# Kernel tuning notes

Hardware: AMD Instinct MI355X
Metric: run time of the kernel (lower is better)

Reference implementation:

```python
import jax, jax.numpy as jnp
import numpy as np

H = 256
EPS = 1e-5
WIN = (-2, -1, 1, 2)  # radius_graph(pos/2^(d+1), k=2) on unit-spaced timestamps


def leaky(x):
    return jnp.where(x >= 0, x, 0.2 * x)


def layernorm(x, g, b):
    mu = jnp.mean(x, axis=-1, keepdims=True)
    var = jnp.mean(jnp.square(x - mu), axis=-1, keepdims=True)
    return (x - mu) * jax.lax.rsqrt(var + EPS) * g + b


def nbr_mean(x, offsets):
    # mean over temporal-window neighbors within each video row; [B,T,C]
    if not offsets:
        return jnp.zeros_like(x)
    T = x.shape[1]
    idx = jnp.arange(T)
    acc = jnp.zeros_like(x)
    cnt = jnp.zeros((T,), x.dtype)
    for o in offsets:
        valid = (idx + o >= 0) & (idx + o < T)
        acc = acc + jnp.where(valid[None, :, None], jnp.roll(x, -o, axis=1), 0.0)
        cnt = cnt + valid.astype(x.dtype)
    return acc / jnp.maximum(cnt, 1.0)[None, :, None]


def conv(x, Ws, Wn, b, offsets):
    # GraphConv with mean aggregation: W_self x_i + W_nbr mean_j x_j + b
    return x @ Ws + nbr_mean(x, offsets) @ Wn + b


def stage(x, s, Wself, Wnbr, bconv, ln_g, ln_b, offsets):
    # Dropout(eval)=id; conv; LeakyReLU(0.2); conv; LayerNorm; LeakyReLU(0.2)
    x = leaky(conv(x, Wself[s, 0], Wnbr[s, 0], bconv[s, 0], offsets))
    x = conv(x, Wself[s, 1], Wnbr[s, 1], bconv[s, 1], offsets)
    return leaky(layernorm(x, ln_g[s], ln_b[s]))


def upsample2(c):
    # knn_interpolate(k=2) from coarse (stride-2 subsampled) grid back to fine grid:
    # even fine nodes coincide with a coarse node (dist 0 -> weight ~inf -> copy);
    # odd fine nodes are equidistant from two coarse nodes (0.5/0.5), except the
    # last odd node whose 2-NN are at dist s and 3s -> weights 0.9/0.1.
    even = c
    nxt = jnp.concatenate([c[:, 1:], c[:, -1:]], axis=1)
    odd = 0.5 * (c + nxt)
    odd = odd.at[:, -1].set(0.9 * c[:, -1] + 0.1 * c[:, -2])
    B, Tc, C = c.shape
    return jnp.stack([even, odd], axis=2).reshape(B, 2 * Tc, C)


def setup_inputs() -> dict:
    key = jax.random.key(0)
    ks = jax.random.split(key, 8)
    B, T, F = 16, 4096, 1024
    N = B * T
    x = jax.random.normal(ks[0], (N, 1, F), dtype=jnp.float32)
    pos = (jnp.arange(N) % T).astype(jnp.float32)
    batch = (jnp.arange(N) // T).astype(jnp.int64)
    indices = (jnp.arange(N) % T).astype(jnp.int64)
    Wp = jax.random.normal(ks[1], (F, H), dtype=jnp.float32) / np.sqrt(F)
    bp = jnp.zeros((H,), jnp.float32)
    Wself = jax.random.normal(ks[2], (6, 2, H, H), dtype=jnp.float32) / np.sqrt(H)
    Wnbr = jax.random.normal(ks[3], (6, 2, H, H), dtype=jnp.float32) / np.sqrt(H)
    bconv = jnp.zeros((6, 2, H), jnp.float32)
    ln_g = jnp.ones((6, H), jnp.float32)
    ln_b = jnp.zeros((6, H), jnp.float32)
    return {"x": x, "pos": pos, "batch": batch, "indices": indices, "B": B, "T": T,
            "Wp": Wp, "bp": bp, "Wself": Wself, "Wnbr": Wnbr, "bconv": bconv,
            "ln_g": ln_g, "ln_b": ln_b}


def reference(x, pos, batch, indices, B, T, Wp, bp, Wself, Wnbr, bconv, ln_g, ln_b):
    # input projection: Rearrange 'B S F -> B (S F)' (S=1) + Linear
    feat = x.reshape(B, T, -1) @ Wp + bp  # [B,T,H]
    # ---- Temporal Encoder ----
    f = feat
    skips = [feat]  # depth-0 input graph features
    for d in range(3):
        f = f[:, ::2]  # batch_subsampling time pooling (stride 2)
        f = f + stage(f, d, Wself, Wnbr, bconv, ln_g, ln_b, WIN)
        if d < 2:
            skips.append(f)
    # ---- Function-Aware Decoder (eval path: clustering_at_inference=False) ----
    for i in range(3):
        res = skips[2 - i]
        f = res + upsample2(f)  # knn_interpolate(k=2) + skip
        dep = 2 - i
        # radius_graph(indices, 1.5): pooled index spacing 2^dep > 1.5 for dep>=1 -> no edges
        offs = WIN if dep == 0 else ()
        f = stage(f, 3 + i, Wself, Wnbr, bconv, ln_g, ln_b, offs)
    return f  # finest-resolution decoder output [B,T,H]
```

## Files before the change

kernel.cpp:

```cpp
#include <hip/hip_runtime.h>

#define HH 256

typedef __attribute__((ext_vector_type(8))) short short8;
typedef __attribute__((ext_vector_type(4))) float f32x4;
typedef __attribute__((ext_vector_type(4))) unsigned short u16x4;
typedef __attribute__((ext_vector_type(8))) unsigned short u16x8;

constexpr int NBATCH = 16;
constexpr int T0   = 4096;
constexpr int FDIM = 1024;
constexpr int R0   = NBATCH * T0;
constexpr int R1   = R0 / 2;
constexpr int R2   = R0 / 4;
constexpr int R3   = R0 / 8;

__device__ __forceinline__ float b2f(unsigned short u) {
    union { unsigned int i; float f; } v; v.i = ((unsigned int)u) << 16; return v.f;
}
__device__ __forceinline__ unsigned short f2b(float f) {
    union { float f; unsigned int i; } v; v.f = f;
    unsigned int r = v.i + 0x7fffu + ((v.i >> 16) & 1u);
    return (unsigned short)(r >> 16);
}
__device__ __forceinline__ void gload16(const void* g, void* l) {
    __builtin_amdgcn_global_load_lds((const __attribute__((address_space(1))) void*)g,
                                     (__attribute__((address_space(3))) void*)l, 16, 0, 0);
}
__device__ __forceinline__ int swz_ks(int chunk)        { return (chunk & 3) ^ ((chunk >> 3) & 3); }
__device__ __forceinline__ int frag_idx(int row, int g) { return (row * 4 + (g ^ ((row >> 1) & 3))) * 8; }

__global__ void transpose_w(const float* __restrict__ src, unsigned short* __restrict__ dst,
                            int K, int tilesPerMat)
{
    int bid = blockIdx.x;
    int m = bid / tilesPerMat;
    int t = bid % tilesPerMat;
    int tr = t >> 3, tc = t & 7;
    const float* S = src + (size_t)m * K * HH;
    unsigned short* D = dst + (size_t)m * HH * K;
    __shared__ float tile[32][33];
    int x = threadIdx.x & 31, y = threadIdx.x >> 5;
#pragma unroll
    for (int i = y; i < 32; i += 8)
        tile[i][x] = S[(size_t)(tr * 32 + i) * HH + tc * 32 + x];
    __syncthreads();
#pragma unroll
    for (int i = y; i < 32; i += 8)
        D[(size_t)(tc * 32 + i) * K + tr * 32 + x] = f2b(tile[x][i]);
}

template<int AMODE, int NBR, int LEAKY>
__launch_bounds__(512)
__global__ void conv_gemm(const unsigned short* __restrict__ A,
                          const unsigned short* __restrict__ Cc,
                          const unsigned short* __restrict__ Bself,
                          const unsigned short* __restrict__ Bnbr,
                          const float* __restrict__ bias,
                          unsigned short* __restrict__ out,
                          int Tl, int Tc, int tlshift)
{
    __shared__ unsigned short As[2][128 * 32];
    __shared__ unsigned short Bs[2][256 * 32];
    const int tid  = threadIdx.x;
    const int lane = tid & 63;
    const int w    = tid >> 6;
    const int wm   = w & 1, wn = w >> 1;
    const long row0 = (long)blockIdx.x * 128;

    const int arr = tid >> 2;
    const int akk = swz_ks(tid);
    const long gr = row0 + arr;

    float ca = 0.f, cb = 0.f; size_t rc0 = 0, rc1 = 0;
    if (AMODE == 2) {
        int t = (int)(gr & (long)(Tl - 1));
        long bq = gr >> tlshift;
        int k = t >> 1;
        rc0 = (size_t)bq * Tc + k;
        if (!(t & 1))        { ca = 1.0f; cb = 0.0f; rc1 = rc0; }
        else if (k < Tc - 1) { ca = 0.5f; cb = 0.5f; rc1 = rc0 + 1; }
        else                 { ca = 0.9f; cb = 0.1f; rc1 = rc0 - 1; }
    }
    int vmask = 0; float vinv = 1.f;
    size_t nrow0 = 0, nrow1 = 0, nrow2 = 0, nrow3 = 0;
    if (NBR) {
        const int offs[4] = {-2, -1, 1, 2};
        int t = (int)(gr & (long)(Tl - 1));
        int cnt = 0;
        size_t nr[4] = {0, 0, 0, 0};
#pragma unroll
        for (int oi = 0; oi < 4; oi++) {
            int tn = t + offs[oi];
            if (tn >= 0 && tn < Tl) {
                vmask |= 1 << oi; cnt++;
                long r = gr + offs[oi];
                nr[oi] = (size_t)((AMODE == 1) ? 2 * r : r) * HH;
            }
        }
        vinv = 1.f / (float)cnt;
        nrow0 = nr[0]; nrow1 = nr[1]; nrow2 = nr[2]; nrow3 = nr[3];
    }

    f32x4 acc[4][4] = {};
    u16x8 pv0 = {}, pv1 = {}, pv2 = {}, pv3 = {};

    const int NT = NBR ? 16 : 8;

    auto issue = [&](int t, int b) {
        const int seg = NBR ? (t >> 3) : 0;
        const int k0 = (t & 7) * 32;
        const unsigned short* __restrict__ Bm = (NBR && seg) ? Bnbr : Bself;
        gload16(Bm + (size_t)arr * HH + k0 + akk * 8,        &Bs[b][tid * 8]);
        gload16(Bm + (size_t)(128 + arr) * HH + k0 + akk * 8, &Bs[b][(tid + 512) * 8]);
        if (seg == 0) {
            if (AMODE == 0) {
                gload16(A + (size_t)gr * HH + k0 + akk * 8, &As[b][tid * 8]);
            } else if (AMODE == 1) {
                gload16(A + (size_t)(2 * gr) * HH + k0 + akk * 8, &As[b][tid * 8]);
            } else {
                pv0 = *(const u16x8*)(A + (size_t)gr * HH + k0 + akk * 8);
                pv1 = *(const u16x8*)(Cc + rc0 * HH + k0 + akk * 8);
                pv2 = *(const u16x8*)(Cc + rc1 * HH + k0 + akk * 8);
            }
        } else {
            if (vmask & 1) pv0 = *(const u16x8*)(A + nrow0 + k0 + akk * 8);
            if (vmask & 2) pv1 = *(const u16x8*)(A + nrow1 + k0 + akk * 8);
            if (vmask & 4) pv2 = *(const u16x8*)(A + nrow2 + k0 + akk * 8);
            if (vmask & 8) pv3 = *(const u16x8*)(A + nrow3 + k0 + akk * 8);
        }
    };
    auto finish = [&](int t, int b) {
        const int seg = NBR ? (t >> 3) : 0;
        if (seg == 0) {
            if (AMODE == 2) {
                u16x8 o;
#pragma unroll
                for (int j = 0; j < 8; j++)
                    o[j] = f2b(b2f(pv0[j]) + ca * b2f(pv1[j]) + cb * b2f(pv2[j]));
                *(u16x8*)&As[b][tid * 8] = o;
            }
        } else {
            float a8[8] = {0, 0, 0, 0, 0, 0, 0, 0};
            if (vmask & 1) {
#pragma unroll
                for (int j = 0; j < 8; j++) a8[j] += b2f(pv0[j]);
            }
            if (vmask & 2) {
#pragma unroll
                for (int j = 0; j < 8; j++) a8[j] += b2f(pv1[j]);
            }
            if (vmask & 4) {
#pragma unroll
                for (int j = 0; j < 8; j++) a8[j] += b2f(pv2[j]);
            }
            if (vmask & 8) {
#pragma unroll
                for (int j = 0; j < 8; j++) a8[j] += b2f(pv3[j]);
            }
            u16x8 o;
#pragma unroll
            for (int j = 0; j < 8; j++) o[j] = f2b(a8[j] * vinv);
            *(u16x8*)&As[b][tid * 8] = o;
        }
    };

    issue(0, 0);
    finish(0, 0);
    __syncthreads();

    int buf = 0;
#pragma unroll
    for (int t = 0; t < NT; ++t) {
        if (t + 1 < NT) issue(t + 1, buf ^ 1);

        short8 af[4], bg[4];
#pragma unroll
        for (int i = 0; i < 4; i++) {
            af[i] = *(const short8*)&As[buf][frag_idx(wm * 64 + i * 16 + (lane & 15), lane >> 4)];
            bg[i] = *(const short8*)&Bs[buf][frag_idx(wn * 64 + i * 16 + (lane & 15), lane >> 4)];
        }
#pragma unroll
        for (int mi = 0; mi < 4; mi++)
#pragma unroll
            for (int ni = 0; ni < 4; ni++)
                acc[mi][ni] = __builtin_amdgcn_mfma_f32_16x16x32_bf16(af[mi], bg[ni], acc[mi][ni], 0, 0, 0);

        if (t + 1 < NT) {
            finish(t + 1, buf ^ 1);
            __syncthreads();
            buf ^= 1;
        }
    }

#pragma unroll
    for (int mi = 0; mi < 4; mi++) {
        size_t rbase = (size_t)row0 + wm * 64 + mi * 16 + (lane >> 4) * 4;
#pragma unroll
        for (int ni = 0; ni < 4; ni++) {
            int c = wn * 64 + ni * 16 + (lane & 15);
            float bb = bias[c];
            f32x4 v = acc[mi][ni];
#pragma unroll
            for (int r = 0; r < 4; r++) {
                float t = v[r] + bb;
                if (LEAKY) t = (t >= 0.f) ? t : 0.2f * t;
                out[(rbase + r) * HH + c] = f2b(t);
            }
        }
    }
}

__launch_bounds__(512)
__global__ void proj_gemm(const float* __restrict__ A, const unsigned short* __restrict__ Bt,
                          const float* __restrict__ bias, unsigned short* __restrict__ out)
{
    __shared__ unsigned short As[2][128 * 32];
    __shared__ unsigned short Bs[2][256 * 32];
    const int tid  = threadIdx.x;
    const int lane = tid & 63;
    const int w    = tid >> 6;
    const int wm   = w & 1, wn = w >> 1;
    const size_t row0 = (size_t)blockIdx.x * 128;

    const int arr = tid >> 2;
    const int akk = swz_ks(tid);

    f32x4 acc[4][4] = {};
    float4 pa0, pa1;

    const int NT = FDIM / 32;

    auto issue = [&](int t, int b) {
        const int k0 = t * 32;
        gload16(Bt + (size_t)arr * FDIM + k0 + akk * 8,         &Bs[b][tid * 8]);
        gload16(Bt + (size_t)(128 + arr) * FDIM + k0 + akk * 8, &Bs[b][(tid + 512) * 8]);
        const float* s = A + (row0 + arr) * (size_t)FDIM + k0 + akk * 8;
        pa0 = *(const float4*)s;
        pa1 = *(const float4*)(s + 4);
    };
    auto finish = [&](int t, int b) {
        u16x8 o = { f2b(pa0.x), f2b(pa0.y), f2b(pa0.z), f2b(pa0.w),
                    f2b(pa1.x), f2b(pa1.y), f2b(pa1.z), f2b(pa1.w) };
        *(u16x8*)&As[b][tid * 8] = o;
    };

    issue(0, 0);
    finish(0, 0);
    __syncthreads();

    int buf = 0;
    for (int t = 0; t < NT; ++t) {
        if (t + 1 < NT) issue(t + 1, buf ^ 1);

        short8 af[4], bg[4];
#pragma unroll
        for (int i = 0; i < 4; i++) {
            af[i] = *(const short8*)&As[buf][frag_idx(wm * 64 + i * 16 + (lane & 15), lane >> 4)];
            bg[i] = *(const short8*)&Bs[buf][frag_idx(wn * 64 + i * 16 + (lane & 15), lane >> 4)];
        }
#pragma unroll
        for (int mi = 0; mi < 4; mi++)
#pragma unroll
            for (int ni = 0; ni < 4; ni++)
                acc[mi][ni] = __builtin_amdgcn_mfma_f32_16x16x32_bf16(af[mi], bg[ni], acc[mi][ni], 0, 0, 0);

        if (t + 1 < NT) {
            finish(t + 1, buf ^ 1);
            __syncthreads();
            buf ^= 1;
        }
    }

#pragma unroll
    for (int mi = 0; mi < 4; mi++) {
        size_t rbase = row0 + wm * 64 + mi * 16 + (lane >> 4) * 4;
#pragma unroll
        for (int ni = 0; ni < 4; ni++) {
            int c = wn * 64 + ni * 16 + (lane & 15);
            float bb = bias[c];
            f32x4 v = acc[mi][ni];
#pragma unroll
            for (int r = 0; r < 4; r++)
                out[(rbase + r) * HH + c] = f2b(v[r] + bb);
        }
    }
}

__global__ void upsample_add_kernel(unsigned short* __restrict__ res, const unsigned short* __restrict__ c,
                                    int Tc, int tlshift, int Rout)
{
    int idx = blockIdx.x * 256 + threadIdx.x;
    int r = idx >> 5, cc = (idx & 31) * 8;
    if (r >= Rout) return;
    int Tl = Tc * 2;
    int t  = r & (Tl - 1);
    int bq = r >> tlshift;
    int k  = t >> 1;
    size_t rc = (size_t)bq * Tc + k;
    float u[8];
    if (!(t & 1)) {
        u16x8 v = *(const u16x8*)(c + rc * HH + cc);
#pragma unroll
        for (int j = 0; j < 8; j++) u[j] = b2f(v[j]);
    } else if (k < Tc - 1) {
        u16x8 v0 = *(const u16x8*)(c + rc * HH + cc);
        u16x8 v1 = *(const u16x8*)(c + (rc + 1) * HH + cc);
#pragma unroll
        for (int j = 0; j < 8; j++) u[j] = 0.5f * (b2f(v0[j]) + b2f(v1[j]));
    } else {
        u16x8 v0 = *(const u16x8*)(c + rc * HH + cc);
        u16x8 vm = *(const u16x8*)(c + (rc - 1) * HH + cc);
#pragma unroll
        for (int j = 0; j < 8; j++) u[j] = 0.9f * b2f(v0[j]) + 0.1f * b2f(vm[j]);
    }
    u16x8 rv = *(const u16x8*)(res + (size_t)r * HH + cc);
    u16x8 o;
#pragma unroll
    for (int j = 0; j < 8; j++) o[j] = f2b(b2f(rv[j]) + u[j]);
    *(u16x8*)(res + (size_t)r * HH + cc) = o;
}

template<int MODE>
__launch_bounds__(256)
__global__ void ln_kernel(const unsigned short* __restrict__ src, void* __restrict__ dstv,
                          const unsigned short* __restrict__ prev,
                          const float* __restrict__ g, const float* __restrict__ b)
{
    size_t row = (size_t)blockIdx.x * 4 + (threadIdx.x >> 6);
    int lane = threadIdx.x & 63;
    u16x4 xv = *(const u16x4*)(src + row * HH + lane * 4);
    float x0 = b2f(xv[0]), x1 = b2f(xv[1]), x2 = b2f(xv[2]), x3 = b2f(xv[3]);

    float s = x0 + x1 + x2 + x3;
#pragma unroll
    for (int off = 32; off >= 1; off >>= 1) s += __shfl_xor(s, off);
    float mu = s * (1.0f / HH);

    float d0 = x0 - mu, d1 = x1 - mu, d2 = x2 - mu, d3 = x3 - mu;
    float vs = d0 * d0 + d1 * d1 + d2 * d2 + d3 * d3;
#pragma unroll
    for (int off = 32; off >= 1; off >>= 1) vs += __shfl_xor(vs, off);
    float inv = rsqrtf(vs * (1.0f / HH) + 1e-5f);

    float4 gv = *reinterpret_cast<const float4*>(g + lane * 4);
    float4 bv = *reinterpret_cast<const float4*>(b + lane * 4);
    float y0 = d0 * inv * gv.x + bv.x;
    float y1 = d1 * inv * gv.y + bv.y;
    float y2 = d2 * inv * gv.z + bv.z;
    float y3 = d3 * inv * gv.w + bv.w;
    y0 = (y0 >= 0.f) ? y0 : 0.2f * y0;
    y1 = (y1 >= 0.f) ? y1 : 0.2f * y1;
    y2 = (y2 >= 0.f) ? y2 : 0.2f * y2;
    y3 = (y3 >= 0.f) ? y3 : 0.2f * y3;

    if (MODE == 2) {
        float* d = (float*)dstv + row * HH + lane * 4;
        *reinterpret_cast<float4*>(d) = make_float4(y0, y1, y2, y3);
    } else {
        if (MODE == 1) {
            u16x4 rv = *(const u16x4*)(prev + (2 * row) * HH + lane * 4);
            y0 += b2f(rv[0]); y1 += b2f(rv[1]); y2 += b2f(rv[2]); y3 += b2f(rv[3]);
        }
        unsigned short* d = (unsigned short*)dstv + row * HH + lane * 4;
        u16x4 o = { f2b(y0), f2b(y1), f2b(y2), f2b(y3) };
        *(u16x4*)d = o;
    }
}

extern "C" void kernel_launch(void* const* d_in, const int* in_sizes, int n_in,
                              void* d_out, int out_size, void* d_ws, size_t ws_size,
                              hipStream_t stream)
{
    const float* x     = (const float*)d_in[0];
    const float* Wp    = (const float*)d_in[6];
    const float* bp    = (const float*)d_in[7];
    const float* Wself = (const float*)d_in[8];
    const float* Wnbr  = (const float*)d_in[9];
    const float* bconv = (const float*)d_in[10];
    const float* ln_g  = (const float*)d_in[11];
    const float* ln_b  = (const float*)d_in[12];
    float* out = (float*)d_out;

    char* p = (char*)d_ws;
    unsigned short* Wself_t = (unsigned short*)p; p += (size_t)12 * HH * HH * 2;
    unsigned short* Wnbr_t  = (unsigned short*)p; p += (size_t)12 * HH * HH * 2;
    unsigned short* Wp_t    = (unsigned short*)p; p += (size_t)HH * FDIM * 2;
    unsigned short* c0 = (unsigned short*)p; p += (size_t)R0 * HH * 2;
    unsigned short* c1 = (unsigned short*)p; p += (size_t)R1 * HH * 2;
    unsigned short* c2 = (unsigned short*)p; p += (size_t)R2 * HH * 2;
    unsigned short* c3 = (unsigned short*)p; p += (size_t)R3 * HH * 2;
    unsigned short* t1 = (unsigned short*)p; p += (size_t)R0 * HH * 2;
    unsigned short* t2 = (unsigned short*)p; p += (size_t)R0 * HH * 2;
    if (ws_size < (size_t)(p - (char*)d_ws)) return;

    auto Ws = [&](int i) { return Wself_t + (size_t)i * HH * HH; };
    auto Wn = [&](int i) { return Wnbr_t  + (size_t)i * HH * HH; };

    transpose_w<<<12 * 64, 256, 0, stream>>>(Wself, Wself_t, HH, 64);
    transpose_w<<<12 * 64, 256, 0, stream>>>(Wnbr,  Wnbr_t,  HH, 64);
    transpose_w<<<256, 256, 0, stream>>>(Wp, Wp_t, FDIM, 256);

    proj_gemm<<<R0 / 128, 512, 0, stream>>>(x, Wp_t, bp, c0);

    conv_gemm<1, 1, 1><<<R1 / 128, 512, 0, stream>>>(c0, nullptr, Ws(0), Wn(0), bconv + 0 * HH, t1, 2048, 0, 0);
    conv_gemm<0, 1, 0><<<R1 / 128, 512, 0, stream>>>(t1, nullptr, Ws(1), Wn(1), bconv + 1 * HH, t2, 2048, 0, 0);
    ln_kernel<1><<<R1 / 4, 256, 0, stream>>>(t2, c1, c0, ln_g + 0 * HH, ln_b + 0 * HH);

    conv_gemm<1, 1, 1><<<R2 / 128, 512, 0, stream>>>(c1, nullptr, Ws(2), Wn(2), bconv + 2 * HH, t1, 1024, 0, 0);
    conv_gemm<0, 1, 0><<<R2 / 128, 512, 0, stream>>>(t1, nullptr, Ws(3), Wn(3), bconv + 3 * HH, t2, 1024, 0, 0);
    ln_kernel<1><<<R2 / 4, 256, 0, stream>>>(t2, c2, c1, ln_g + 1 * HH, ln_b + 1 * HH);

    conv_gemm<1, 1, 1><<<R3 / 128, 512, 0, stream>>>(c2, nullptr, Ws(4), Wn(4), bconv + 4 * HH, t1, 512, 0, 0);
    conv_gemm<0, 1, 0><<<R3 / 128, 512, 0, stream>>>(t1, nullptr, Ws(5), Wn(5), bconv + 5 * HH, t2, 512, 0, 0);
    ln_kernel<1><<<R3 / 4, 256, 0, stream>>>(t2, c3, c2, ln_g + 2 * HH, ln_b + 2 * HH);

    conv_gemm<2, 0, 1><<<R2 / 128, 512, 0, stream>>>(c2, c3, Ws(6), nullptr, bconv + 6 * HH, t1, 1024, 512, 10);
    conv_gemm<0, 0, 0><<<R2 / 128, 512, 0, stream>>>(t1, nullptr, Ws(7), nullptr, bconv + 7 * HH, t2, 1024, 0, 0);
    ln_kernel<0><<<R2 / 4, 256, 0, stream>>>(t2, c2, nullptr, ln_g + 3 * HH, ln_b + 3 * HH);
    conv_gemm<2, 0, 1><<<R1 / 128, 512, 0, stream>>>(c1, c2, Ws(8), nullptr, bconv + 8 * HH, t1, 2048, 1024, 11);
    conv_gemm<0, 0, 0><<<R1 / 128, 512, 0, stream>>>(t1, nullptr, Ws(9), nullptr, bconv + 9 * HH, t2, 2048, 0, 0);
    ln_kernel<0><<<R1 / 4, 256, 0, stream>>>(t2, c1, nullptr, ln_g + 4 * HH, ln_b + 4 * HH);
    upsample_add_kernel<<<R0 / 8, 256, 0, stream>>>(c0, c1, 2048, 12, R0);
    conv_gemm<0, 1, 1><<<R0 / 128, 512, 0, stream>>>(c0, nullptr, Ws(10), Wn(10), bconv + 10 * HH, t1, 4096, 0, 0);
    conv_gemm<0, 1, 0><<<R0 / 128, 512, 0, stream>>>(t1, nullptr, Ws(11), Wn(11), bconv + 11 * HH, t2, 4096, 0, 0);
    ln_kernel<2><<<R0 / 4, 256, 0, stream>>>(t2, out, nullptr, ln_g + 5 * HH, ln_b + 5 * HH);
}
```

Before: 430.5 us.

## Fuse LayerNorm into second conv GEMM epilogue and triple-buffer K pipeline

Removes the standalone LayerNorm kernel by computing row mean and variance in the second conv GEMM's epilogue, using cross-lane shuffles plus a small LDS reduction across the four N-waves. The residual add and final fp32 output are written directly, which drops the t2 intermediate round trip. GEMM mainloops move from double to triple buffering with explicit vmcnt waits and raw barriers, and raise wave priority around the MFMA block. Neighbour gathers become branchless by clamping indices and applying validity coefficients. Risks include higher LDS use lowering occupancy, a single-pass variance formula that can lose precision, and brittle hand-written waitcnt counts.

```diff
diff --git a/kernel.cpp b/kernel.cpp
--- a/kernel.cpp
+++ b/kernel.cpp
@@ -27,8 +27,22 @@
     __builtin_amdgcn_global_load_lds((const __attribute__((address_space(1))) void*)g,
                                      (__attribute__((address_space(3))) void*)l, 16, 0, 0);
 }
+__device__ __forceinline__ void barrier_sync() {
+    asm volatile("s_waitcnt lgkmcnt(0)\n\ts_barrier" ::: "memory");
+}
+__device__ __forceinline__ void wait_vm(int n) {
+    switch (n) {
+    case 3: asm volatile("s_waitcnt vmcnt(3)" ::: "memory"); break;
+    case 4: asm volatile("s_waitcnt vmcnt(4)" ::: "memory"); break;
+    case 5: asm volatile("s_waitcnt vmcnt(5)" ::: "memory"); break;
+    case 6: asm volatile("s_waitcnt vmcnt(6)" ::: "memory"); break;
+    default: asm volatile("s_waitcnt vmcnt(0)" ::: "memory"); break;
+    }
+}
 __device__ __forceinline__ int swz_ks(int chunk)        { return (chunk & 3) ^ ((chunk >> 3) & 3); }
 __device__ __forceinline__ int frag_idx(int row, int g) { return (row * 4 + (g ^ ((row >> 1) & 3))) * 8; }
+
+struct PVv { u16x8 v0, v1, v2, v3; };
 
 __global__ void transpose_w(const float* __restrict__ src, unsigned short* __restrict__ dst,
                             int K, int tilesPerMat)
@@ -50,18 +64,24 @@
         D[(size_t)(tc * 32 + i) * K + tr * 32 + x] = f2b(tile[x][i]);
 }
 
-template<int AMODE, int NBR, int LEAKY>
+template<int AMODE, int NBR, int LNFUSE, int OUT>
 __launch_bounds__(512)
-__global__ void conv_gemm(const unsigned short* __restrict__ A,
-                          const unsigned short* __restrict__ Cc,
-                          const unsigned short* __restrict__ Bself,
-                          const unsigned short* __restrict__ Bnbr,
-                          const float* __restrict__ bias,
-                          unsigned short* __restrict__ out,
-                          int Tl, int Tc, int tlshift)
+__global__ void conv_fused(const unsigned short* __restrict__ A,
+                           const unsigned short* __restrict__ Cc,
+                           const unsigned short* __restrict__ prev,
+                           const unsigned short* __restrict__ Bself,
+                           const unsigned short* __restrict__ Bnbr,
+                           const float* __restrict__ bias,
+                           const float* __restrict__ lng,
+                           const float* __restrict__ lnb,
+                           void* __restrict__ dstv,
+                           int Tl, int Tc, int tlshift)
 {
-    __shared__ unsigned short As[2][128 * 32];
-    __shared__ unsigned short Bs[2][256 * 32];
+    constexpr int NT = NBR ? 16 : 8;
+    __shared__ unsigned short As[3][128 * 32];
+    __shared__ unsigned short Bs[3][256 * 32];
+    __shared__ float lnred[LNFUSE ? 128 : 1][8];
+
     const int tid  = threadIdx.x;
     const int lane = tid & 63;
     const int w    = tid >> 6;
@@ -82,130 +102,200 @@
         else if (k < Tc - 1) { ca = 0.5f; cb = 0.5f; rc1 = rc0 + 1; }
         else                 { ca = 0.9f; cb = 0.1f; rc1 = rc0 - 1; }
     }
-    int vmask = 0; float vinv = 1.f;
+    float vinv = 1.f;
+    float cf0 = 0.f, cf1 = 0.f, cf2 = 0.f, cf3 = 0.f;
     size_t nrow0 = 0, nrow1 = 0, nrow2 = 0, nrow3 = 0;
     if (NBR) {
         const int offs[4] = {-2, -1, 1, 2};
         int t = (int)(gr & (long)(Tl - 1));
         int cnt = 0;
-        size_t nr[4] = {0, 0, 0, 0};
+        float cf[4]; size_t nr[4];
 #pragma unroll
         for (int oi = 0; oi < 4; oi++) {
             int tn = t + offs[oi];
-            if (tn >= 0 && tn < Tl) {
-                vmask |= 1 << oi; cnt++;
-                long r = gr + offs[oi];
-                nr[oi] = (size_t)((AMODE == 1) ? 2 * r : r) * HH;
-            }
+            bool v = (tn >= 0 && tn < Tl);
+            cnt += v ? 1 : 0;
+            int tcl = tn < 0 ? 0 : (tn > Tl - 1 ? Tl - 1 : tn);
+            long r = gr - t + tcl;
+            nr[oi] = (size_t)((AMODE == 1) ? 2 * r : r) * HH;
+            cf[oi] = v ? 1.f : 0.f;
         }
         vinv = 1.f / (float)cnt;
+        cf0 = cf[0]; cf1 = cf[1]; cf2 = cf[2]; cf3 = cf[3];
         nrow0 = nr[0]; nrow1 = nr[1]; nrow2 = nr[2]; nrow3 = nr[3];
     }
 
     f32x4 acc[4][4] = {};
-    u16x8 pv0 = {}, pv1 = {}, pv2 = {}, pv3 = {};
-
-    const int NT = NBR ? 16 : 8;
-
-    auto issue = [&](int t, int b) {
-        const int seg = NBR ? (t >> 3) : 0;
+    PVv pvE = {}, pvO = {};
+
+    auto Lof = [&](int t) -> int {
+        const int seg = (NBR && t >= 8) ? 1 : 0;
+        return seg ? 6 : (AMODE == 2 ? 5 : 3);
+    };
+    auto issueB = [&](int t) {
+        const int seg = (NBR && t >= 8) ? 1 : 0;
         const int k0 = (t & 7) * 32;
-        const unsigned short* __restrict__ Bm = (NBR && seg) ? Bnbr : Bself;
-        gload16(Bm + (size_t)arr * HH + k0 + akk * 8,        &Bs[b][tid * 8]);
-        gload16(Bm + (size_t)(128 + arr) * HH + k0 + akk * 8, &Bs[b][(tid + 512) * 8]);
+        const int sl = t % 3;
+        const unsigned short* __restrict__ Bm = seg ? Bnbr : Bself;
+        gload16(Bm + (size_t)arr * HH + k0 + akk * 8,         &Bs[sl][tid * 8]);
+        gload16(Bm + (size_t)(128 + arr) * HH + k0 + akk * 8, &Bs[sl][(tid + 512) * 8]);
+    };
+    auto issueA = [&](int t, PVv& pv) {
+        const int seg = (NBR && t >= 8) ? 1 : 0;
+        const int k0 = (t & 7) * 32;
+        const int sl = t % 3;
         if (seg == 0) {
             if (AMODE == 0) {
-                gload16(A + (size_t)gr * HH + k0 + akk * 8, &As[b][tid * 8]);
+                gload16(A + (size_t)gr * HH + k0 + akk * 8, &As[sl][tid * 8]);
             } else if (AMODE == 1) {
-                gload16(A + (size_t)(2 * gr) * HH + k0 + akk * 8, &As[b][tid * 8]);
+                gload16(A + (size_t)(2 * gr) * HH + k0 + akk * 8, &As[sl][tid * 8]);
             } else {
-                pv0 = *(const u16x8*)(A + (size_t)gr * HH + k0 + akk * 8);
-                pv1 = *(const u16x8*)(Cc + rc0 * HH + k0 + akk * 8);
-                pv2 = *(const u16x8*)(Cc + rc1 * HH + k0 + akk * 8);
+                pv.v0 = *(const u16x8*)(A + (size_t)gr * HH + k0 + akk * 8);
+                pv.v1 = *(const u16x8*)(Cc + rc0 * HH + k0 + akk * 8);
+                pv.v2 = *(const u16x8*)(Cc + rc1 * HH + k0 + akk * 8);
             }
         } else {
-            if (vmask & 1) pv0 = *(const u16x8*)(A + nrow0 + k0 + akk * 8);
-            if (vmask & 2) pv1 = *(const u16x8*)(A + nrow1 + k0 + akk * 8);
-            if (vmask & 4) pv2 = *(const u16x8*)(A + nrow2 + k0 + akk * 8);
-            if (vmask & 8) pv3 = *(const u16x8*)(A + nrow3 + k0 + akk * 8);
-        }
-    };
-    auto finish = [&](int t, int b) {
-        const int seg = NBR ? (t >> 3) : 0;
+            pv.v0 = *(const u16x8*)(A + nrow0 + k0 + akk * 8);
+            pv.v1 = *(const u16x8*)(A + nrow1 + k0 + akk * 8);
+            pv.v2 = *(const u16x8*)(A + nrow2 + k0 + akk * 8);
+            pv.v3 = *(const u16x8*)(A + nrow3 + k0 + akk * 8);
+        }
+    };
+    auto finishA = [&](int t, PVv& pv) {
+        const int seg = (NBR && t >= 8) ? 1 : 0;
+        const int sl = t % 3;
         if (seg == 0) {
             if (AMODE == 2) {
                 u16x8 o;
 #pragma unroll
                 for (int j = 0; j < 8; j++)
-                    o[j] = f2b(b2f(pv0[j]) + ca * b2f(pv1[j]) + cb * b2f(pv2[j]));
-                *(u16x8*)&As[b][tid * 8] = o;
+                    o[j] = f2b(b2f(pv.v0[j]) + ca * b2f(pv.v1[j]) + cb * b2f(pv.v2[j]));
+                *(u16x8*)&As[sl][tid * 8] = o;
             }
         } else {
-            float a8[8] = {0, 0, 0, 0, 0, 0, 0, 0};
-            if (vmask & 1) {
-#pragma unroll
-                for (int j = 0; j < 8; j++) a8[j] += b2f(pv0[j]);
-            }
-            if (vmask & 2) {
-#pragma unroll
-                for (int j = 0; j < 8; j++) a8[j] += b2f(pv1[j]);
-            }
-            if (vmask & 4) {
-#pragma unroll
-                for (int j = 0; j < 8; j++) a8[j] += b2f(pv2[j]);
-            }
-            if (vmask & 8) {
-#pragma unroll
-                for (int j = 0; j < 8; j++) a8[j] += b2f(pv3[j]);
-            }
             u16x8 o;
 #pragma unroll
-            for (int j = 0; j < 8; j++) o[j] = f2b(a8[j] * vinv);
-            *(u16x8*)&As[b][tid * 8] = o;
-        }
-    };
-
-    issue(0, 0);
-    finish(0, 0);
-    __syncthreads();
-
-    int buf = 0;
+            for (int j = 0; j < 8; j++) {
+                float a = cf0 * b2f(pv.v0[j]) + cf1 * b2f(pv.v1[j])
+                        + cf2 * b2f(pv.v2[j]) + cf3 * b2f(pv.v3[j]);
+                o[j] = f2b(a * vinv);
+            }
+            *(u16x8*)&As[sl][tid * 8] = o;
+        }
+    };
+
+    issueB(0); issueA(0, pvE);
+    issueB(1); issueA(1, pvO);
+    wait_vm(Lof(1));
+    finishA(0, pvE);
+    barrier_sync();
+
 #pragma unroll
     for (int t = 0; t < NT; ++t) {
-        if (t + 1 < NT) issue(t + 1, buf ^ 1);
-
+        if (t + 2 < NT) {
+            issueB(t + 2);
+            if (((t + 2) & 1) == 0) issueA(t + 2, pvE); else issueA(t + 2, pvO);
+        }
+
+        const int sl = t % 3;
+        __builtin_amdgcn_s_setprio(1);
         short8 af[4], bg[4];
 #pragma unroll
         for (int i = 0; i < 4; i++) {
-            af[i] = *(const short8*)&As[buf][frag_idx(wm * 64 + i * 16 + (lane & 15), lane >> 4)];
-            bg[i] = *(const short8*)&Bs[buf][frag_idx(wn * 64 + i * 16 + (lane & 15), lane >> 4)];
+            af[i] = *(const short8*)&As[sl][frag_idx(wm * 64 + i * 16 + (lane & 15), lane >> 4)];
+            bg[i] = *(const short8*)&Bs[sl][frag_idx(wn * 64 + i * 16 + (lane & 15), lane >> 4)];
         }
 #pragma unroll
         for (int mi = 0; mi < 4; mi++)
 #pragma unroll
             for (int ni = 0; ni < 4; ni++)
                 acc[mi][ni] = __builtin_amdgcn_mfma_f32_16x16x32_bf16(af[mi], bg[ni], acc[mi][ni], 0, 0, 0);
+        __builtin_amdgcn_s_setprio(0);
 
         if (t + 1 < NT) {
-            finish(t + 1, buf ^ 1);
-            __syncthreads();
-            buf ^= 1;
-        }
-    }
-
-#pragma unroll
-    for (int mi = 0; mi < 4; mi++) {
-        size_t rbase = (size_t)row0 + wm * 64 + mi * 16 + (lane >> 4) * 4;
+            wait_vm((t + 2 < NT) ? Lof(t + 2) : 0);
+            if (((t + 1) & 1) == 0) finishA(t + 1, pvE); else finishA(t + 1, pvO);
+            barrier_sync();
+        }
+    }
+
+    if (LNFUSE == 0) {
+        unsigned short* outp = (unsigned short*)dstv;
+#pragma unroll
+        for (int mi = 0; mi < 4; mi++) {
+            size_t rbase = (size_t)row0 + wm * 64 + mi * 16 + (lane >> 4) * 4;
+#pragma unroll
+            for (int ni = 0; ni < 4; ni++) {
+                int c = wn * 64 + ni * 16 + (lane & 15);
+                float bb = bias[c];
+                f32x4 v = acc[mi][ni];
+#pragma unroll
+                for (int r = 0; r < 4; r++) {
+                    float t = v[r] + bb;
+                    t = (t >= 0.f) ? t : 0.2f * t;
+                    outp[(rbase + r) * HH + c] = f2b(t);
+                }
+            }
+        }
+    } else {
+        float bb[4];
+#pragma unroll
+        for (int ni = 0; ni < 4; ni++) bb[ni] = bias[wn * 64 + ni * 16 + (lane & 15)];
+
+#pragma unroll
+        for (int mi = 0; mi < 4; mi++) {
+#pragma unroll
+            for (int r = 0; r < 4; r++) {
+                float s = 0.f, q = 0.f;
+#pragma unroll
+                for (int ni = 0; ni < 4; ni++) {
+                    float v = acc[mi][ni][r] + bb[ni];
+                    s += v; q += v * v;
+                }
+                s += __shfl_xor(s, 1); q += __shfl_xor(q, 1);
+                s += __shfl_xor(s, 2); q += __shfl_xor(q, 2);
+                s += __shfl_xor(s, 4); q += __shfl_xor(q, 4);
+                s += __shfl_xor(s, 8); q += __shfl_xor(q, 8);
+                if ((lane & 15) == 0) {
+                    int row = wm * 64 + mi * 16 + (lane >> 4) * 4 + r;
+                    lnred[row][wn]     = s;
+                    lnred[row][4 + wn] = q;
+                }
+            }
+        }
+        __syncthreads();
+
+        float gv[4], bv[4];
 #pragma unroll
         for (int ni = 0; ni < 4; ni++) {
             int c = wn * 64 + ni * 16 + (lane & 15);
-            float bb = bias[c];
-            f32x4 v = acc[mi][ni];
+            gv[ni] = lng[c]; bv[ni] = lnb[c];
+        }
+
+#pragma unroll
+        for (int mi = 0; mi < 4; mi++) {
 #pragma unroll
             for (int r = 0; r < 4; r++) {
-                float t = v[r] + bb;
-                if (LEAKY) t = (t >= 0.f) ? t : 0.2f * t;
-                out[(rbase + r) * HH + c] = f2b(t);
+                int row = wm * 64 + mi * 16 + (lane >> 4) * 4 + r;
+                float s = lnred[row][0] + lnred[row][1] + lnred[row][2] + lnred[row][3];
+                float q = lnred[row][4] + lnred[row][5] + lnred[row][6] + lnred[row][7];
+                float mu  = s * (1.0f / HH);
+                float var = q * (1.0f / HH) - mu * mu;
+                float inv = rsqrtf(var + 1e-5f);
+                size_t grow = (size_t)row0 + row;
+#pragma unroll
+                for (int ni = 0; ni < 4; ni++) {
+                    int c = wn * 64 + ni * 16 + (lane & 15);
+                    float v = acc[mi][ni][r] + bb[ni];
+                    float y = (v - mu) * inv * gv[ni] + bv[ni];
+                    y = (y >= 0.f) ? y : 0.2f * y;
+                    if (OUT == 2) {
+                        ((float*)dstv)[grow * HH + c] = y;
+                    } else {
+                        if (OUT == 1) y += b2f(prev[(2 * grow) * HH + c]);
+                        ((unsigned short*)dstv)[grow * HH + c] = f2b(y);
+                    }
+                }
             }
         }
     }
@@ -215,8 +305,9 @@
 __global__ void proj_gemm(const float* __restrict__ A, const unsigned short* __restrict__ Bt,
                           const float* __restrict__ bias, unsigned short* __restrict__ out)
 {
-    __shared__ unsigned short As[2][128 * 32];
-    __shared__ unsigned short Bs[2][256 * 32];
+    constexpr int NT = FDIM / 32;
+    __shared__ unsigned short As[3][128 * 32];
+    __shared__ unsigned short Bs[3][256 * 32];
     const int tid  = threadIdx.x;
     const int lane = tid & 63;
     const int w    = tid >> 6;
@@ -227,48 +318,55 @@
     const int akk = swz_ks(tid);
 
     f32x4 acc[4][4] = {};
-    float4 pa0, pa1;
-
-    const int NT = FDIM / 32;
-
-    auto issue = [&](int t, int b) {
+    float4 paE0, paE1, paO0, paO1;
+
+    auto issue = [&](int t, float4& p0, float4& p1) {
         const int k0 = t * 32;
-        gload16(Bt + (size_t)arr * FDIM + k0 + akk * 8,         &Bs[b][tid * 8]);
-        gload16(Bt + (size_t)(128 + arr) * FDIM + k0 + akk * 8, &Bs[b][(tid + 512) * 8]);
+        const int sl = t % 3;
+        gload16(Bt + (size_t)arr * FDIM + k0 + akk * 8,         &Bs[sl][tid * 8]);
+        gload16(Bt + (size_t)(128 + arr) * FDIM + k0 + akk * 8, &Bs[sl][(tid + 512) * 8]);
         const float* s = A + (row0 + arr) * (size_t)FDIM + k0 + akk * 8;
-        pa0 = *(const float4*)s;
-        pa1 = *(const float4*)(s + 4);
-    };
-    auto finish = [&](int t, int b) {
-        u16x8 o = { f2b(pa0.x), f2b(pa0.y), f2b(pa0.z), f2b(pa0.w),
-                    f2b(pa1.x), f2b(pa1.y), f2b(pa1.z), f2b(pa1.w) };
-        *(u16x8*)&As[b][tid * 8] = o;
-    };
-
-    issue(0, 0);
-    finish(0, 0);
-    __syncthreads();
-
-    int buf = 0;
+        p0 = *(const float4*)s;
+        p1 = *(const float4*)(s + 4);
+    };
+    auto finish = [&](int t, float4& p0, float4& p1) {
+        const int sl = t % 3;
+        u16x8 o = { f2b(p0.x), f2b(p0.y), f2b(p0.z), f2b(p0.w),
+                    f2b(p1.x), f2b(p1.y), f2b(p1.z), f2b(p1.w) };
+        *(u16x8*)&As[sl][tid * 8] = o;
+    };
+
+    issue(0, paE0, paE1);
+    issue(1, paO0, paO1);
+    wait_vm(4);
+    finish(0, paE0, paE1);
+    barrier_sync();
+
+#pragma unroll
     for (int t = 0; t < NT; ++t) {
-        if (t + 1 < NT) issue(t + 1, buf ^ 1);
-
+        if (t + 2 < NT) {
+            if (((t + 2) & 1) == 0) issue(t + 2, paE0, paE1); else issue(t + 2, paO0, paO1);
+        }
+
+        const int sl = t % 3;
+        __builtin_amdgcn_s_setprio(1);
         short8 af[4], bg[4];
 #pragma unroll
         for (int i = 0; i < 4; i++) {
-            af[i] = *(const short8*)&As[buf][frag_idx(wm * 64 + i * 16 + (lane & 15), lane >> 4)];
-            bg[i] = *(const short8*)&Bs[buf][frag_idx(wn * 64 + i * 16 + (lane & 15), lane >> 4)];
+            af[i] = *(const short8*)&As[sl][frag_idx(wm * 64 + i * 16 + (lane & 15), lane >> 4)];
+            bg[i] = *(const short8*)&Bs[sl][frag_idx(wn * 64 + i * 16 + (lane & 15), lane >> 4)];
         }
 #pragma unroll
         for (int mi = 0; mi < 4; mi++)
 #pragma unroll
             for (int ni = 0; ni < 4; ni++)
                 acc[mi][ni] = __builtin_amdgcn_mfma_f32_16x16x32_bf16(af[mi], bg[ni], acc[mi][ni], 0, 0, 0);
+        __builtin_amdgcn_s_setprio(0);
 
         if (t + 1 < NT) {
-            finish(t + 1, buf ^ 1);
-            __syncthreads();
-            buf ^= 1;
+            wait_vm((t + 2 < NT) ? 4 : 0);
+            if (((t + 1) & 1) == 0) finish(t + 1, paE0, paE1); else finish(t + 1, paO0, paO1);
+            barrier_sync();
         }
     }
 
@@ -321,53 +419,6 @@
     *(u16x8*)(res + (size_t)r * HH + cc) = o;
 }
 
-template<int MODE>
-__launch_bounds__(256)
-__global__ void ln_kernel(const unsigned short* __restrict__ src, void* __restrict__ dstv,
-                          const unsigned short* __restrict__ prev,
-                          const float* __restrict__ g, const float* __restrict__ b)
-{
-    size_t row = (size_t)blockIdx.x * 4 + (threadIdx.x >> 6);
-    int lane = threadIdx.x & 63;
-    u16x4 xv = *(const u16x4*)(src + row * HH + lane * 4);
-    float x0 = b2f(xv[0]), x1 = b2f(xv[1]), x2 = b2f(xv[2]), x3 = b2f(xv[3]);
-
-    float s = x0 + x1 + x2 + x3;
-#pragma unroll
-    for (int off = 32; off >= 1; off >>= 1) s += __shfl_xor(s, off);
-    float mu = s * (1.0f / HH);
-
-    float d0 = x0 - mu, d1 = x1 - mu, d2 = x2 - mu, d3 = x3 - mu;
-    float vs = d0 * d0 + d1 * d1 + d2 * d2 + d3 * d3;
-#pragma unroll
-    for (int off = 32; off >= 1; off >>= 1) vs += __shfl_xor(vs, off);
-    float inv = rsqrtf(vs * (1.0f / HH) + 1e-5f);
-
-    float4 gv = *reinterpret_cast<const float4*>(g + lane * 4);
-    float4 bv = *reinterpret_cast<const float4*>(b + lane * 4);
-    float y0 = d0 * inv * gv.x + bv.x;
-    float y1 = d1 * inv * gv.y + bv.y;
-    float y2 = d2 * inv * gv.z + bv.z;
-    float y3 = d3 * inv * gv.w + bv.w;
-    y0 = (y0 >= 0.f) ? y0 : 0.2f * y0;
-    y1 = (y1 >= 0.f) ? y1 : 0.2f * y1;
-    y2 = (y2 >= 0.f) ? y2 : 0.2f * y2;
-    y3 = (y3 >= 0.f) ? y3 : 0.2f * y3;
-
-    if (MODE == 2) {
-        float* d = (float*)dstv + row * HH + lane * 4;
-        *reinterpret_cast<float4*>(d) = make_float4(y0, y1, y2, y3);
-    } else {
-        if (MODE == 1) {
-            u16x4 rv = *(const u16x4*)(prev + (2 * row) * HH + lane * 4);
-            y0 += b2f(rv[0]); y1 += b2f(rv[1]); y2 += b2f(rv[2]); y3 += b2f(rv[3]);
-        }
-        unsigned short* d = (unsigned short*)dstv + row * HH + lane * 4;
-        u16x4 o = { f2b(y0), f2b(y1), f2b(y2), f2b(y3) };
-        *(u16x4*)d = o;
-    }
-}
-
 extern "C" void kernel_launch(void* const* d_in, const int* in_sizes, int n_in,
                               void* d_out, int out_size, void* d_ws, size_t ws_size,
                               hipStream_t stream)
@@ -391,7 +442,6 @@
     unsigned short* c2 = (unsigned short*)p; p += (size_t)R2 * HH * 2;
     unsigned short* c3 = (unsigned short*)p; p += (size_t)R3 * HH * 2;
     unsigned short* t1 = (unsigned short*)p; p += (size_t)R0 * HH * 2;
-    unsigned short* t2 = (unsigned short*)p; p += (size_t)R0 * HH * 2;
     if (ws_size < (size_t)(p - (char*)d_ws)) return;
 
     auto Ws = [&](int i) { return Wself_t + (size_t)i * HH * HH; };
@@ -403,26 +453,34 @@
 
     proj_gemm<<<R0 / 128, 512, 0, stream>>>(x, Wp_t, bp, c0);
 
-    conv_gemm<1, 1, 1><<<R1 / 128, 512, 0, stream>>>(c0, nullptr, Ws(0), Wn(0), bconv + 0 * HH, t1, 2048, 0, 0);
-    conv_gemm<0, 1, 0><<<R1 / 128, 512, 0, stream>>>(t1, nullptr, Ws(1), Wn(1), bconv + 1 * HH, t2, 2048, 0, 0);
-    ln_kernel<1><<<R1 / 4, 256, 0, stream>>>(t2, c1, c0, ln_g + 0 * HH, ln_b + 0 * HH);
-
-    conv_gemm<1, 1, 1><<<R2 / 128, 512, 0, stream>>>(c1, nullptr, Ws(2), Wn(2), bconv + 2 * HH, t1, 1024, 0, 0);
-    conv_gemm<0, 1, 0><<<R2 / 128, 512, 0, stream>>>(t1, nullptr, Ws(3), Wn(3), bconv + 3 * HH, t2, 1024, 0, 0);
-    ln_kernel<1><<<R2 / 4, 256, 0, stream>>>(t2, c2, c1, ln_g + 1 * HH, ln_b + 1 * HH);
-
-    conv_gemm<1, 1, 1><<<R3 / 128, 512, 0, stream>>>(c2, nullptr, Ws(4), Wn(4), bconv + 4 * HH, t1, 512, 0, 0);
-    conv_gemm<0, 1, 0><<<R3 / 128, 512, 0, stream>>>(t1, nullptr, Ws(5), Wn(5), bconv + 5 * HH, t2, 512, 0, 0);
-    ln_kernel<1><<<R3 / 4, 256, 0, stream>>>(t2, c3, c2, ln_g + 2 * HH, ln_b + 2 * HH);
-
-    conv_gemm<2, 0, 1><<<R2 / 128, 512, 0, stream>>>(c2, c3, Ws(6), nullptr, bconv + 6 * HH, t1, 1024, 512, 10);
-    conv_gemm<0, 0, 0><<<R2 / 128, 512, 0, stream>>>(t1, nullptr, Ws(7), nullptr, bconv + 7 * HH, t2, 1024, 0, 0);
-    ln_kernel<0><<<R2 / 4, 256, 0, stream>>>(t2, c2, nullptr, ln_g + 3 * HH, ln_b + 3 * HH);
-    conv_gemm<2, 0, 1><<<R1 / 128, 512, 0, stream>>>(c1, c2, Ws(8), nullptr, bconv + 8 * HH, t1, 2048, 1024, 11);
-    conv_gemm<0, 0, 0><<<R1 / 128, 512, 0, stream>>>(t1, nullptr, Ws(9), nullptr, bconv + 9 * HH, t2, 2048, 0, 0);
-    ln_kernel<0><<<R1 / 4, 256, 0, stream>>>(t2, c1, nullptr, ln_g + 4 * HH, ln_b + 4 * HH);
+    conv_fused<1, 1, 0, 0><<<R1 / 128, 512, 0, stream>>>(c0, nullptr, nullptr, Ws(0), Wn(0),
+        bconv + 0 * HH, nullptr, nullptr, t1, 2048, 0, 0);
+    conv_fused<0, 1, 1, 1><<<R1 / 128, 512, 0, stream>>>(t1, nullptr, c0, Ws(1), Wn(1),
+        bconv + 1 * HH, ln_g + 0 * HH, ln_b + 0 * HH, c1, 2048, 0, 0);
+
+    conv_fused<1, 1, 0, 0><<<R2 / 128, 512, 0, stream>>>(c1, nullptr, nullptr, Ws(2), Wn(2),
+        bconv + 2 * HH, nullptr, nullptr, t1, 1024, 0, 0);
+    conv_fused<0, 1, 1, 1><<<R2 / 128, 512, 0, stream>>>(t1, nullptr, c1, Ws(3), Wn(3),
+        bconv + 3 * HH, ln_g + 1 * HH, ln_b + 1 * HH, c2, 1024, 0, 0);
+
+    conv_fused<1, 1, 0, 0><<<R3 / 128, 512, 0, stream>>>(c2, nullptr, nullptr, Ws(4), Wn(4),
+        bconv + 4 * HH, nullptr, nullptr, t1, 512, 0, 0);
+    conv_fused<0, 1, 1, 1><<<R3 / 128, 512, 0, stream>>>(t1, nullptr, c2, Ws(5), Wn(5),
+        bconv + 5 * HH, ln_g + 2 * HH, ln_b + 2 * HH, c3, 512, 0, 0);
+
+    conv_fused<2, 0, 0, 0><<<R2 / 128, 512, 0, stream>>>(c2, c3, nullptr, Ws(6), nullptr,
+        bconv + 6 * HH, nullptr, nullptr, t1, 1024, 512, 10);
+    conv_fused<0, 0, 1, 0><<<R2 / 128, 512, 0, stream>>>(t1, nullptr, nullptr, Ws(7), nullptr,
+        bconv + 7 * HH, ln_g + 3 * HH, ln_b + 3 * HH, c2, 1024, 0, 0);
+
+    conv_fused<2, 0, 0, 0><<<R1 / 128, 512, 0, stream>>>(c1, c2, nullptr, Ws(8), nullptr,
+        bconv + 8 * HH, nullptr, nullptr, t1, 2048, 1024, 11);
+    conv_fused<0, 0, 1, 0><<<R1 / 128, 512, 0, stream>>>(t1, nullptr, nullptr, Ws(9), nullptr,
+        bconv + 9 * HH, ln_g + 4 * HH, ln_b + 4 * HH, c1, 2048, 0, 0);
+
     upsample_add_kernel<<<R0 / 8, 256, 0, stream>>>(c0, c1, 2048, 12, R0);
-    conv_gemm<0, 1, 1><<<R0 / 128, 512, 0, stream>>>(c0, nullptr, Ws(10), Wn(10), bconv + 10 * HH, t1, 4096, 0, 0);
-    conv_gemm<0, 1, 0><<<R0 / 128, 512, 0, stream>>>(t1, nullptr, Ws(11), Wn(11), bconv + 11 * HH, t2, 4096, 0, 0);
-    ln_kernel<2><<<R0 / 4, 256, 0, stream>>>(t2, out, nullptr, ln_g + 5 * HH, ln_b + 5 * HH);
-}
+    conv_fused<0, 1, 0, 0><<<R0 / 128, 512, 0, stream>>>(c0, nullptr, nullptr, Ws(10), Wn(10),
+        bconv + 10 * HH, nullptr, nullptr, t1, 4096, 0, 0);
+    conv_fused<0, 1, 1, 2><<<R0 / 128, 512, 0, stream>>>(t1, nullptr, nullptr, Ws(11), Wn(11),
+        bconv + 11 * HH, ln_g + 5 * HH, ln_b + 5 * HH, out, 4096, 0, 0);
+}
```

After: 392.1 us. 8.9% less time.
